# Performance work log

Measured on AMD Instinct MI355X. Metric: run time of the kernel, lower is better.

The kernel has to match this reference:

```python
import jax, jax.numpy as jnp
import numpy as np

D_MODEL = 1024
N_HEADS = 16


def setup_inputs() -> dict:
    key = jax.random.key(0)
    ks = jax.random.split(key, 5)
    B, T, C = 4, 2048, D_MODEL
    x = jax.random.normal(ks[0], (B, T, C), dtype=jnp.float32)
    s = 1.0 / np.sqrt(C)
    W_attn = jax.random.normal(ks[1], (C, 3 * C), dtype=jnp.float32) * s
    b_attn = jnp.zeros((3 * C,), dtype=jnp.float32)
    W_proj = jax.random.normal(ks[2], (C, C), dtype=jnp.float32) * s
    b_proj = jnp.zeros((C,), dtype=jnp.float32)
    return {"x": x, "W_attn": W_attn, "b_attn": b_attn, "W_proj": W_proj, "b_proj": b_proj}


def reference(x, W_attn, b_attn, W_proj, b_proj):
    B, T, C = x.shape
    H = N_HEADS
    hd = C // H
    qkv = x @ W_attn + b_attn                      # [B,T,3C]
    q, k, v = jnp.split(qkv, 3, axis=-1)
    # reshape to [B,H,T,hd]
    q = q.reshape(B, T, H, hd).transpose(0, 2, 1, 3)
    k = k.reshape(B, T, H, hd).transpose(0, 2, 1, 3)
    v = v.reshape(B, T, H, hd).transpose(0, 2, 1, 3)
    scale = 1.0 / jnp.sqrt(jnp.asarray(hd, dtype=x.dtype))
    aff = jnp.einsum('bhqd,bhkd->bhqk', q, k) * scale   # [B,H,T,T]
    causal = jnp.tril(jnp.ones((T, T), dtype=bool))
    aff = jnp.where(causal, aff, jnp.asarray(-jnp.inf, dtype=aff.dtype))
    p = jax.nn.softmax(aff, axis=-1)
    y = jnp.einsum('bhqk,bhkd->bhqd', p, v)             # [B,H,T,hd]
    y = y.transpose(0, 2, 1, 3).reshape(B, T, C)
    return y @ W_proj + b_proj
```

## Files before the change

### kernel.cpp

```cpp
#include <hip/hip_runtime.h>
#include <stdint.h>
#include <math.h>

typedef __attribute__((ext_vector_type(8))) __bf16 bf16x8;
typedef __attribute__((ext_vector_type(4))) __bf16 bf16x4;
typedef __attribute__((ext_vector_type(4))) float f32x4;

#define MFMA16(A, B, C) __builtin_amdgcn_mfma_f32_16x16x32_bf16((A), (B), (C), 0, 0, 0)

#if defined(__has_builtin)
#if __has_builtin(__builtin_amdgcn_exp2f)
#define EXP2(x) __builtin_amdgcn_exp2f(x)
#else
#define EXP2(x) exp2f(x)
#endif
#else
#define EXP2(x) exp2f(x)
#endif

static constexpr int kT  = 2048;
static constexpr int kC  = 1024;
static constexpr int kHD = 64;
#define QSCALE 0.1803368801111204f

__device__ __forceinline__ void g2l16(const void* g, void* l) {
  __builtin_amdgcn_global_load_lds(
      (const __attribute__((address_space(1))) uint32_t*)g,
      (__attribute__((address_space(3))) uint32_t*)l, 16, 0, 0);
}

__global__ __launch_bounds__(256) void k_convert_x(const float* __restrict__ x,
                                                   __bf16* __restrict__ xb) {
  int i = (blockIdx.x * 256 + threadIdx.x) * 4;
  f32x4 v = *(const f32x4*)(x + i);
  bf16x4 o;
  o[0] = (__bf16)v[0]; o[1] = (__bf16)v[1]; o[2] = (__bf16)v[2]; o[3] = (__bf16)v[3];
  *(bf16x4*)(xb + i) = o;
}

__global__ __launch_bounds__(256) void k_transpose_w(const float* __restrict__ src,
                                                     __bf16* __restrict__ dst, int N) {
  __shared__ float t[32][33];
  int k0 = blockIdx.x * 32, n0 = blockIdx.y * 32;
  int c = threadIdx.x & 31, r = threadIdx.x >> 5;
#pragma unroll
  for (int i = 0; i < 4; ++i)
    t[r + i * 8][c] = src[(size_t)(k0 + r + i * 8) * N + n0 + c];
  __syncthreads();
#pragma unroll
  for (int i = 0; i < 4; ++i)
    dst[(size_t)(n0 + r + i * 8) * 1024 + k0 + c] = (__bf16)t[c][r + i * 8];
}

__global__ __launch_bounds__(256) void k_transpose_v(const __bf16* __restrict__ src,
                                                     __bf16* __restrict__ dst) {
  __shared__ __bf16 t[32][33];
  const int t0 = blockIdx.x * 32, d0 = blockIdx.y * 32;
  const size_t base = (size_t)blockIdx.z * kT * kHD;
  int c = threadIdx.x & 31, r = threadIdx.x >> 5;
#pragma unroll
  for (int i = 0; i < 4; ++i)
    t[r + i * 8][c] = src[base + (size_t)(t0 + r + i * 8) * kHD + d0 + c];
  __syncthreads();
#pragma unroll
  for (int i = 0; i < 4; ++i)
    dst[base + (size_t)(d0 + r + i * 8) * kT + t0 + c] = t[c][r + i * 8];
}

template <int MODE>
__global__ __launch_bounds__(256) void k_gemm(const __bf16* __restrict__ A,
                                              const __bf16* __restrict__ Bw,
                                              const float* __restrict__ bias,
                                              __bf16* __restrict__ qo,
                                              __bf16* __restrict__ ko,
                                              __bf16* __restrict__ vo,
                                              float* __restrict__ out) {
  constexpr int K = 1024;
  __shared__ __bf16 As[128 * 64];
  __shared__ __bf16 Bs[128 * 64];
  const int tid = threadIdx.x;
  const int wave = tid >> 6, lane = tid & 63;
  const int lo = lane & 15, hi = lane >> 4;
  const int wm = (wave & 1) * 64, wn = (wave >> 1) * 64;
  const int m0 = blockIdx.y * 128, n0 = blockIdx.x * 128;

  f32x4 acc[4][4] = {};

  const __bf16* ga = A + (size_t)(m0 + wave * 32 + (lane >> 3)) * K + (lane & 7) * 8;
  const __bf16* gb = Bw + (size_t)(n0 + wave * 32 + (lane >> 3)) * K + (lane & 7) * 8;
  __bf16* la = As + wave * 32 * 64;
  __bf16* lb = Bs + wave * 32 * 64;

  for (int kt = 0; kt < K; kt += 64) {
#pragma unroll
    for (int i = 0; i < 4; ++i) {
      g2l16(ga + (size_t)i * 8 * K + kt, la + i * 8 * 64);
      g2l16(gb + (size_t)i * 8 * K + kt, lb + i * 8 * 64);
    }
    __syncthreads();
#pragma unroll
    for (int kk = 0; kk < 64; kk += 32) {
      bf16x8 af[4], bfr[4];
#pragma unroll
      for (int i = 0; i < 4; ++i)
        af[i] = *(const bf16x8*)&As[(wm + i * 16 + lo) * 64 + kk + hi * 8];
#pragma unroll
      for (int j = 0; j < 4; ++j)
        bfr[j] = *(const bf16x8*)&Bs[(wn + j * 16 + lo) * 64 + kk + hi * 8];
#pragma unroll
      for (int i = 0; i < 4; ++i)
#pragma unroll
        for (int j = 0; j < 4; ++j)
          acc[i][j] = MFMA16(af[i], bfr[j], acc[i][j]);
    }
    __syncthreads();
  }

  if (MODE == 0) {
#pragma unroll
    for (int j = 0; j < 4; ++j) {
      int gn = n0 + wn + j * 16 + lo;
      float bv = bias[gn];
      int which = gn >> 10;
      int c = gn & 1023;
      int hh = c >> 6, d = c & 63;
#pragma unroll
      for (int i = 0; i < 4; ++i) {
        int gm = m0 + wm + i * 16 + hi * 4;
#pragma unroll
        for (int r = 0; r < 4; ++r) {
          int m = gm + r;
          int bb = m >> 11, t = m & 2047;
          float val = acc[i][j][r] + bv;
          size_t idx = (((size_t)(bb * 16 + hh)) * 2048 + t) * 64 + d;
          if (which == 0)
            qo[idx] = (__bf16)(val * QSCALE);
          else if (which == 1)
            ko[idx] = (__bf16)val;
          else
            vo[idx] = (__bf16)val;
        }
      }
    }
  } else {
#pragma unroll
    for (int j = 0; j < 4; ++j) {
      int gn = n0 + wn + j * 16 + lo;
      float bv = bias[gn];
#pragma unroll
      for (int i = 0; i < 4; ++i) {
        int gm = m0 + wm + i * 16 + hi * 4;
#pragma unroll
        for (int r = 0; r < 4; ++r)
          out[(size_t)(gm + r) * 1024 + gn] = acc[i][j][r] + bv;
      }
    }
  }
}

__global__ __launch_bounds__(256, 4) void k_flash(const __bf16* __restrict__ qb,
                                                  const __bf16* __restrict__ kb,
                                                  const __bf16* __restrict__ vt,
                                                  __bf16* __restrict__ ob) {
  __shared__ __bf16 Ks[64 * 64];
  __shared__ __bf16 Vs[64 * 64];
  __shared__ __bf16 Ps[4][16 * 68];

  const int id = (int)blockIdx.y * 16 + (int)blockIdx.x;
  const int xcd = id & 7, jj = id >> 3;
  const int bh = (jj & 7) * 8 + xcd;
  const int xs = jj >> 3;
  const int b = bh >> 4, h = bh & 15;
  const int tid = threadIdx.x, wave = tid >> 6, lane = tid & 63;
  const int lo = lane & 15, hi = lane >> 4;

  const int qrow[2] = { (31 - xs) * 64 + wave * 16, xs * 64 + wave * 16 };

  bf16x8 qf[2][2];
#pragma unroll
  for (int rg = 0; rg < 2; ++rg) {
    const __bf16* Qp = qb + ((size_t)bh * kT + qrow[rg]) * kHD;
    qf[rg][0] = *(const bf16x8*)(Qp + lo * kHD + hi * 8);
    qf[rg][1] = *(const bf16x8*)(Qp + lo * kHD + 32 + hi * 8);
  }

  bf16x8 onesf;
#pragma unroll
  for (int e = 0; e < 8; ++e) onesf[e] = (lo == 0) ? (__bf16)1.0f : (__bf16)0.0f;

  f32x4 acc[2][4] = {};
  f32x4 accsum[2] = {};

  const __bf16* Kbase = kb + (size_t)bh * kT * kHD;
  const __bf16* Vbase = vt + (size_t)bh * kHD * kT;

  int srcK[2], srcV[2];
#pragma unroll
  for (int p = 0; p < 2; ++p) {
    int g = wave * 64 + lane + p * 256;
    int r = g >> 3, c = g & 7;
    int cs = c ^ (r & 7);
    srcK[p] = r * kHD + cs * 8;
    srcV[p] = r * kT + cs * 8;
  }
  const int sw0 = (hi ^ (lo & 7)) * 8;
  const int sw1 = ((hi + 4) ^ (lo & 7)) * 8;

  const int nt = 32 - xs;
  for (int it = 0; it < nt; ++it) {
    const int kt = it * 64;
    const bool both = (it <= xs);

#pragma unroll
    for (int p = 0; p < 2; ++p) {
      g2l16(Kbase + kt * kHD + srcK[p], Ks + wave * 512 + p * 2048);
      g2l16(Vbase + kt + srcV[p],       Vs + wave * 512 + p * 2048);
    }
    __syncthreads();

    f32x4 s[2][4];
#pragma unroll
    for (int j = 0; j < 4; ++j) {
      const int row = (j * 16 + lo) * 64;
      bf16x8 kf0 = *(const bf16x8*)&Ks[row + sw0];
      bf16x8 kf1 = *(const bf16x8*)&Ks[row + sw1];
      f32x4 z = {};
      z = MFMA16(qf[0][0], kf0, z);
      z = MFMA16(qf[0][1], kf1, z);
      s[0][j] = z;
      if (both) {
        f32x4 z1 = {};
        z1 = MFMA16(qf[1][0], kf0, z1);
        z1 = MFMA16(qf[1][1], kf1, z1);
        s[1][j] = z1;
      }
    }

    bf16x8 pf[2][2];
#pragma unroll
    for (int rg = 0; rg < 2; ++rg) {
      if (rg == 1 && !both) break;
      const int q0 = qrow[rg] + hi * 4;
      if (kt + 63 > q0) {
#pragma unroll
        for (int j = 0; j < 4; ++j)
#pragma unroll
          for (int r = 0; r < 4; ++r)
            if (kt + j * 16 + lo > q0 + r) s[rg][j][r] = -INFINITY;
      }
#pragma unroll
      for (int j = 0; j < 4; ++j)
#pragma unroll
        for (int r = 0; r < 4; ++r)
          s[rg][j][r] = EXP2(s[rg][j][r]);
      __bf16* Pw = &Ps[wave][0];
#pragma unroll
      for (int j = 0; j < 4; ++j)
#pragma unroll
        for (int r = 0; r < 4; ++r)
          Pw[(hi * 4 + r) * 68 + j * 16 + lo] = (__bf16)s[rg][j][r];
      pf[rg][0] = *(const bf16x8*)&Pw[lo * 68 + hi * 8];
      pf[rg][1] = *(const bf16x8*)&Pw[lo * 68 + 32 + hi * 8];
    }

    accsum[0] = MFMA16(pf[0][0], onesf, accsum[0]);
    accsum[0] = MFMA16(pf[0][1], onesf, accsum[0]);
    if (both) {
      accsum[1] = MFMA16(pf[1][0], onesf, accsum[1]);
      accsum[1] = MFMA16(pf[1][1], onesf, accsum[1]);
    }
#pragma unroll
    for (int jd = 0; jd < 4; ++jd) {
      const int row = (jd * 16 + lo) * 64;
      bf16x8 vf0 = *(const bf16x8*)&Vs[row + sw0];
      bf16x8 vf1 = *(const bf16x8*)&Vs[row + sw1];
      acc[0][jd] = MFMA16(pf[0][0], vf0, acc[0][jd]);
      acc[0][jd] = MFMA16(pf[0][1], vf1, acc[0][jd]);
      if (both) {
        acc[1][jd] = MFMA16(pf[1][0], vf0, acc[1][jd]);
        acc[1][jd] = MFMA16(pf[1][1], vf1, acc[1][jd]);
      }
    }
    __syncthreads();
  }

#pragma unroll
  for (int rg = 0; rg < 2; ++rg) {
    float inv[4];
#pragma unroll
    for (int r = 0; r < 4; ++r)
      inv[r] = 1.0f / __shfl(accsum[rg][r], hi * 16, 64);
    __bf16* Op = ob + ((size_t)b * kT + qrow[rg]) * kC + h * kHD;
#pragma unroll
    for (int jd = 0; jd < 4; ++jd)
#pragma unroll
      for (int r = 0; r < 4; ++r)
        Op[(hi * 4 + r) * kC + jd * 16 + lo] = (__bf16)(acc[rg][jd][r] * inv[r]);
  }
}

extern "C" void kernel_launch(void* const* d_in, const int* in_sizes, int n_in,
                              void* d_out, int out_size, void* d_ws, size_t ws_size,
                              hipStream_t stream) {
  const float* x      = (const float*)d_in[0];
  const float* W_attn = (const float*)d_in[1];
  const float* b_attn = (const float*)d_in[2];
  const float* W_proj = (const float*)d_in[3];
  const float* b_proj = (const float*)d_in[4];
  float* out = (float*)d_out;

  char* ws = (char*)d_ws;
  __bf16* xb  = (__bf16*)(ws + 0);
  __bf16* vtb = (__bf16*)(ws + 0);
  __bf16* wab = (__bf16*)(ws + 16777216);
  __bf16* wpb = (__bf16*)(ws + 23068672);
  __bf16* qbf = (__bf16*)(ws + 25165824);
  __bf16* kbf = (__bf16*)(ws + 41943040);
  __bf16* vbf = (__bf16*)(ws + 58720256);
  __bf16* ob  = (__bf16*)(ws + 58720256);

  k_convert_x<<<8192, 256, 0, stream>>>(x, xb);
  k_transpose_w<<<dim3(32, 96), 256, 0, stream>>>(W_attn, wab, 3072);
  k_transpose_w<<<dim3(32, 32), 256, 0, stream>>>(W_proj, wpb, 1024);
  k_gemm<0><<<dim3(24, 64), 256, 0, stream>>>(xb, wab, b_attn, qbf, kbf, vbf, nullptr);
  k_transpose_v<<<dim3(64, 2, 64), 256, 0, stream>>>(vbf, vtb);
  k_flash<<<dim3(16, 64), 256, 0, stream>>>(qbf, kbf, vtb, ob);
  k_gemm<1><<<dim3(8, 64), 256, 0, stream>>>(ob, wpb, b_proj, nullptr, nullptr, nullptr, out);
}
```

Measured before the change: 292.9 us.

## Double-buffer K/V tiles in flash kernel and swizzle P scratch buffer

Splits the K and V shared-memory tiles into two buffers. The next tile's global-to-LDS copy is issued right after the per-iteration barrier, so it overlaps the current tile's QK, softmax and PV work, and the trailing barrier is dropped. The per-wave P staging buffer also moves from 68-element row padding to a 64-wide XOR-swizzled layout to avoid LDS bank conflicts. Total LDS per block grows to about 40KB, which could limit occupancy against the 4-blocks-per-CU launch bound.

```diff
diff --git a/kernel.cpp b/kernel.cpp
--- a/kernel.cpp
+++ b/kernel.cpp
@@ -162,9 +162,9 @@
                                                   const __bf16* __restrict__ kb,
                                                   const __bf16* __restrict__ vt,
                                                   __bf16* __restrict__ ob) {
-  __shared__ __bf16 Ks[64 * 64];
-  __shared__ __bf16 Vs[64 * 64];
-  __shared__ __bf16 Ps[4][16 * 68];
+  __shared__ __bf16 Ks[2][64 * 64];
+  __shared__ __bf16 Vs[2][64 * 64];
+  __shared__ __bf16 Ps[4][16 * 64];
 
   const int id = (int)blockIdx.y * 16 + (int)blockIdx.x;
   const int xcd = id & 7, jj = id >> 3;
@@ -205,25 +205,41 @@
   }
   const int sw0 = (hi ^ (lo & 7)) * 8;
   const int sw1 = ((hi + 4) ^ (lo & 7)) * 8;
+  const int psw0 = (hi ^ (lo >> 1)) * 8;
+  const int psw1 = ((hi + 4) ^ (lo >> 1)) * 8;
 
   const int nt = 32 - xs;
+
+#pragma unroll
+  for (int p = 0; p < 2; ++p) {
+    g2l16(Kbase + srcK[p], &Ks[0][wave * 512 + p * 2048]);
+    g2l16(Vbase + srcV[p], &Vs[0][wave * 512 + p * 2048]);
+  }
+
   for (int it = 0; it < nt; ++it) {
     const int kt = it * 64;
+    const int pb = it & 1;
     const bool both = (it <= xs);
 
-#pragma unroll
-    for (int p = 0; p < 2; ++p) {
-      g2l16(Kbase + kt * kHD + srcK[p], Ks + wave * 512 + p * 2048);
-      g2l16(Vbase + kt + srcV[p],       Vs + wave * 512 + p * 2048);
-    }
     __syncthreads();
 
+    if (it + 1 < nt) {
+      const int kn = kt + 64;
+#pragma unroll
+      for (int p = 0; p < 2; ++p) {
+        g2l16(Kbase + kn * kHD + srcK[p], &Ks[1 - pb][wave * 512 + p * 2048]);
+        g2l16(Vbase + kn + srcV[p],       &Vs[1 - pb][wave * 512 + p * 2048]);
+      }
+    }
+
+    const __bf16* Kt = &Ks[pb][0];
+    const __bf16* Vt = &Vs[pb][0];
     f32x4 s[2][4];
 #pragma unroll
     for (int j = 0; j < 4; ++j) {
       const int row = (j * 16 + lo) * 64;
-      bf16x8 kf0 = *(const bf16x8*)&Ks[row + sw0];
-      bf16x8 kf1 = *(const bf16x8*)&Ks[row + sw1];
+      bf16x8 kf0 = *(const bf16x8*)&Kt[row + sw0];
+      bf16x8 kf1 = *(const bf16x8*)&Kt[row + sw1];
       f32x4 z = {};
       z = MFMA16(qf[0][0], kf0, z);
       z = MFMA16(qf[0][1], kf1, z);
@@ -257,10 +273,13 @@
 #pragma unroll
       for (int j = 0; j < 4; ++j)
 #pragma unroll
-        for (int r = 0; r < 4; ++r)
-          Pw[(hi * 4 + r) * 68 + j * 16 + lo] = (__bf16)s[rg][j][r];
-      pf[rg][0] = *(const bf16x8*)&Pw[lo * 68 + hi * 8];
-      pf[rg][1] = *(const bf16x8*)&Pw[lo * 68 + 32 + hi * 8];
+        for (int r = 0; r < 4; ++r) {
+          const int q = hi * 4 + r;
+          Pw[q * 64 + (((j * 2 + (lo >> 3)) ^ (q >> 1)) * 8) + (lo & 7)] =
+              (__bf16)s[rg][j][r];
+        }
+      pf[rg][0] = *(const bf16x8*)&Pw[lo * 64 + psw0];
+      pf[rg][1] = *(const bf16x8*)&Pw[lo * 64 + psw1];
     }
 
     accsum[0] = MFMA16(pf[0][0], onesf, accsum[0]);
@@ -272,8 +291,8 @@
 #pragma unroll
     for (int jd = 0; jd < 4; ++jd) {
       const int row = (jd * 16 + lo) * 64;
-      bf16x8 vf0 = *(const bf16x8*)&Vs[row + sw0];
-      bf16x8 vf1 = *(const bf16x8*)&Vs[row + sw1];
+      bf16x8 vf0 = *(const bf16x8*)&Vt[row + sw0];
+      bf16x8 vf1 = *(const bf16x8*)&Vt[row + sw1];
       acc[0][jd] = MFMA16(pf[0][0], vf0, acc[0][jd]);
       acc[0][jd] = MFMA16(pf[0][1], vf1, acc[0][jd]);
       if (both) {
@@ -281,7 +300,6 @@
         acc[1][jd] = MFMA16(pf[1][1], vf1, acc[1][jd]);
       }
     }
-    __syncthreads();
   }
 
 #pragma unroll
```

Result: faster. 285.4 us (-2.5%).
